# Kernel tuning notes

Hardware: AMD Instinct MI355X
Metric: run time of the kernel (lower is better)

## Reference

```python
import jax, jax.numpy as jnp
import numpy as np

LR, AT, DSBETA, EPS_DS = 0.3, 0.9, 1e-4, 0.01


def setup_inputs() -> dict:
    key = jax.random.key(0)
    k1, k2, k3, k4, k5 = jax.random.split(key, 5)
    B, K, D = 8192, 4096, 512
    # 0.25 scale -> squared distances small enough that act_max straddles the 0.9 threshold
    return {
        "input": jax.random.normal(k1, (B, D), jnp.float32) * 0.25,
        "weights": jax.random.normal(k2, (K, D), jnp.float32) * 0.25,
        "moving_avg": jax.random.uniform(k3, (K, D), jnp.float32),
        "relevance": jax.random.uniform(k4, (K, D), jnp.float32),
        "node_control": jax.random.randint(k5, (K,), 0, 2).astype(jnp.float32),
    }


def _forward(input, weights, moving_avg, relevance, node_control):
    B, D = input.shape
    K = weights.shape[0]
    # activation: relevance-weighted pairwise sq-distance
    rel_sum = relevance.sum(1)                                   # [K]
    d = ((input ** 2).sum(1)[:, None] + (weights ** 2).sum(1)[None, :]
         - 2.0 * input @ weights.T)                              # [B,K]
    dw = d * (rel_sum / D)[None, :]
    dw = jnp.where(jnp.isnan(dw), 0.0, dw)
    act = rel_sum[None, :] / (rel_sum[None, :] + dw + 1e-7)      # [B,K]
    act_max = act.max(1)
    idx = jnp.argmax(act, 1)                                     # BMU per sample
    high = act_max >= AT                                         # [B]

    # ---- high-activation branch: segment-mean EMA update of winning nodes ----
    hi = high.astype(input.dtype)
    cnt = jax.ops.segment_sum(hi, idx, num_segments=K)           # [K]
    sums = jax.ops.segment_sum(input * hi[:, None], idx, num_segments=K)
    upd = cnt > 0                                                # nodes that won >=1 high sample
    mean_k = sums / jnp.where(upd, cnt, 1.0)[:, None]            # per-node mean sample
    dist_abs = jnp.abs(mean_k - weights)
    a = LR * DSBETA
    ma1 = jnp.where(upd[:, None], a * dist_abs + (1.0 - a) * moving_avg, moving_avg)
    mx = ma1.max(1, keepdims=True)
    mn = ma1.min(1, keepdims=True)
    av = ma1.mean(1, keepdims=True)
    rel_new = 1.0 / (1.0 + jnp.exp((ma1 - av) / (EPS_DS * (mx - mn))))
    rel1 = jnp.where(upd[:, None], rel_new, relevance)
    delta = LR * (mean_k - weights)
    w1 = jnp.where(upd[:, None], weights + delta, weights)
    nc1 = jnp.where(upd, 1.0, node_control)
    loss = (delta * upd[:, None]).sum() / B

    # ---- low-activation branch: add_node -> copy segment means into free slots ----
    lo = (~high).astype(input.dtype)
    cnt_l = jax.ops.segment_sum(lo, idx, num_segments=K)
    sums_l = jax.ops.segment_sum(input * lo[:, None], idx, num_segments=K)
    low_valid = cnt_l > 0
    low_mean = sums_l / jnp.where(low_valid, cnt_l, 1.0)[:, None]
    avail = nc1 == 0
    n_new = low_valid.sum()
    n_avail = avail.sum()
    n_create = jnp.minimum(n_new, n_avail)
    # torch.unique returns sorted node ids; stable argsort puts valid ids first ascending
    low_order = jnp.argsort(jnp.where(low_valid, 0, 1))          # [K]
    avail_order = jnp.argsort(jnp.where(avail, 0, 1))            # [K]
    r = jnp.arange(K)
    # add_node takes the LAST n_create new samples, fills FIRST n_create free slots
    src = low_order[jnp.clip(n_new - n_create + r, 0, K - 1)]
    vals = low_mean[src]                                         # [K,D]
    wm = r < n_create                                            # write mask per rank
    slot = avail_order                                           # permutation of [K]
    w2 = w1.at[slot].set(jnp.where(wm[:, None], vals, w1[slot]))
    ma2 = ma1.at[slot].set(jnp.where(wm[:, None], 0.0, ma1[slot]))
    rel2 = rel1.at[slot].set(jnp.where(wm[:, None], 1.0, rel1[slot]))
    nc2 = nc1.at[slot].set(jnp.where(wm, 1.0, nc1[slot]))

    state = jnp.stack([w2, ma2, rel2], axis=0)                   # [3,K,D]
    return loss, state, nc2


def reference(input, weights, moving_avg, relevance, node_control):
    return _forward(input, weights, moving_avg, relevance, node_control)
```

## Files before the change

### kernel.cpp

```cpp
#include <hip/hip_runtime.h>

typedef unsigned short ushort_t;
typedef unsigned int uint_t;
typedef __bf16 bf16x8 __attribute__((ext_vector_type(8)));
typedef float f32x4 __attribute__((ext_vector_type(4)));

#define BM 128
#define BN 128

static constexpr float LRC  = 0.3f;
static constexpr float AC   = (float)(0.3 * 1e-4);
static constexpr float OMAC = (float)(1.0 - 0.3 * 1e-4);
static constexpr float EPSC = 0.01f;
static constexpr float ATC  = 0.9f;
static constexpr float DELTA = 5e-4f;

__device__ __forceinline__ void gll16(const void* g, void* l) {
    __builtin_amdgcn_global_load_lds((__attribute__((address_space(1))) void*)g,
                                     (__attribute__((address_space(3))) void*)l,
                                     16, 0, 0);
}

__device__ __forceinline__ ushort_t f2bf_rne(float f) {
    uint_t u = __float_as_uint(f);
    uint_t r = u + 0x7fffu + ((u >> 16) & 1u);
    return (ushort_t)(r >> 16);
}

__global__ __launch_bounds__(128) void k_prep(
    const float* __restrict__ X, const float* __restrict__ W,
    const float* __restrict__ REL,
    ushort_t* __restrict__ Xh, ushort_t* __restrict__ Wh,
    float* __restrict__ xsq, float* __restrict__ wsq, float* __restrict__ rel_sum,
    int B, int D)
{
    int blk = blockIdx.x, t = threadIdx.x;
    bool isX = blk < B;
    int row = isX ? blk : blk - B;
    const float4* src = (const float4*)((isX ? X : W) + (size_t)row * D);
    const float4* rr  = isX ? nullptr : (const float4*)(REL + (size_t)row * D);
    ushort_t* H = isX ? Xh : Wh;
    float q = 0.f, r = 0.f;
    for (int i = t; i < (D >> 2); i += 128) {
        float4 v = src[i];
        if (!isX) { float4 rv = rr[i]; r += rv.x + rv.y + rv.z + rv.w; }
        float x[4] = {v.x, v.y, v.z, v.w};
        ushort_t h[4];
#pragma unroll
        for (int j = 0; j < 4; j++) { q += x[j] * x[j]; h[j] = f2bf_rne(x[j]); }
        ((ushort4*)H)[(size_t)row * (D >> 2) + i] = make_ushort4(h[0], h[1], h[2], h[3]);
    }
    __shared__ float s1[128], s2[128];
    s1[t] = q; s2[t] = r; __syncthreads();
    for (int off = 64; off > 0; off >>= 1) {
        if (t < off) { s1[t] += s1[t + off]; s2[t] += s2[t + off]; }
        __syncthreads();
    }
    if (t == 0) {
        if (isX) xsq[row] = s1[0];
        else { wsq[row] = s1[0]; rel_sum[row] = s2[0]; }
    }
}

__global__ __launch_bounds__(256, 2) void k_gemm_act(
    const ushort_t* __restrict__ Xh, const ushort_t* __restrict__ Wh,
    const float* __restrict__ xsq, const float* __restrict__ wsq,
    const float* __restrict__ rs,
    float* __restrict__ tmaxA, int* __restrict__ cntA,
    float* __restrict__ actsA, int* __restrict__ idxsA,
    int K, int D)
{
    __shared__ char smem[26624];

    const int tid = threadIdx.x;
    const int wave = tid >> 6, lane = tid & 63;
    const int nk = K / BN;
    const int bx = blockIdx.x % nk, by = blockIdx.x / nk;
    const int b0 = by * BM, k0 = bx * BN;

    const int srow = wave * 32 + (lane >> 2);
    const int schunk = ((lane & 3) - (lane >> 3)) & 3;
    const int scol = schunk * 8;
    const size_t gx = (size_t)(b0 + srow) * D + scol;
    const size_t gw = (size_t)(k0 + srow) * D + scol;
    const size_t c1 = (size_t)16 * D;
    char* lb = smem + wave * 2048;

    const int wm = wave >> 1, wn = wave & 1;
    const int l15 = lane & 15, quad = lane >> 4;
    const int roff = (l15 * 4 + ((quad + (l15 >> 1)) & 3)) * 16;
    const int aoff = (wm * 4) * 1024 + roff;
    const int boff = (wn * 4) * 1024 + roff;

    f32x4 acc[4][4];
#pragma unroll
    for (int i = 0; i < 4; i++)
#pragma unroll
        for (int j = 0; j < 4; j++) acc[i][j] = (f32x4){0.f, 0.f, 0.f, 0.f};

    for (int kd = 0; kd < D; kd += 32) {
        gll16(Xh + gx + kd,      lb + 0);
        gll16(Xh + gx + c1 + kd, lb + 1024);
        gll16(Wh + gw + kd,      lb + 8192);
        gll16(Wh + gw + c1 + kd, lb + 8192 + 1024);
        __syncthreads();

        bf16x8 ah[4], bh[4];
#pragma unroll
        for (int t = 0; t < 4; t++) {
            ah[t] = *(const bf16x8*)(smem + 0    + aoff + t * 1024);
            bh[t] = *(const bf16x8*)(smem + 8192 + boff + t * 1024);
        }
#pragma unroll
        for (int j = 0; j < 4; j++)
#pragma unroll
            for (int i = 0; i < 4; i++)
                acc[i][j] = __builtin_amdgcn_mfma_f32_16x16x32_bf16(ah[i], bh[j], acc[i][j], 0, 0, 0);
        __syncthreads();
    }

    float rsv[4], wqv[4], epsors[4];
#pragma unroll
    for (int tn = 0; tn < 4; tn++) {
        int c = k0 + wn * 64 + tn * 16 + l15;
        float rv = rs[c];
        rsv[tn] = rv; wqv[tn] = wsq[c];
        epsors[tn] = 1e-7f / rv;
    }
    const float invD = 1.f / (float)D;
    float* redM    = (float*)smem;
    float* tmaxrow = (float*)(smem + 16896);
    float* thrqrow = (float*)(smem + 17408);
    int*   cntL    = (int*)(smem + 17920);
    float* lsActs  = (float*)(smem + 18432);
    int*   lsIdx   = (int*)(smem + 22528);

#pragma unroll
    for (int tm = 0; tm < 4; tm++) {
#pragma unroll
        for (int r = 0; r < 4; r++) {
            int rowl = wm * 64 + tm * 16 + quad * 4 + r;
            float xq = xsq[b0 + rowl];
            float qmin = 1e30f;
#pragma unroll
            for (int tn = 0; tn < 4; tn++) {
                float dd = (xq + wqv[tn]) - 2.f * acc[tm][tn][r];
                float q = dd * invD + epsors[tn];
                acc[tm][tn][r] = q;
                qmin = fminf(qmin, q);
            }
            redM[rowl * 33 + wn * 16 + l15] = qmin;
        }
    }
    __syncthreads();
    if (tid < BM) {
        float qm = 1e30f;
#pragma unroll
        for (int t2 = 0; t2 < 32; t2++) qm = fminf(qm, redM[tid * 33 + t2]);
        float tmax = 1.f / (1.f + qm);
        tmaxrow[tid] = tmax;
        thrqrow[tid] = 1.f / (tmax - DELTA) - 1.f;
        cntL[tid] = 0;
    }
    __syncthreads();
#pragma unroll
    for (int tm = 0; tm < 4; tm++) {
#pragma unroll
        for (int r = 0; r < 4; r++) {
            int rowl = wm * 64 + tm * 16 + quad * 4 + r;
            float tq = thrqrow[rowl];
#pragma unroll
            for (int tn = 0; tn < 4; tn++) {
                float q = acc[tm][tn][r];
                if (q <= tq) {
                    int pos = atomicAdd(&cntL[rowl], 1);
                    if (pos < 8) {
                        lsActs[rowl * 8 + pos] = 1.f / (1.f + q);
                        lsIdx[rowl * 8 + pos]  = k0 + wn * 64 + tn * 16 + l15;
                    }
                }
            }
        }
    }
    __syncthreads();
    if (tid < BM) {
        size_t base = (size_t)(b0 + tid) * nk + bx;
        tmaxA[base] = tmaxrow[tid];
        int c = cntL[tid];
        cntA[base] = c;
        int cc = c < 8 ? c : 8;
        for (int s = 0; s < cc; s++) {
            actsA[base * 8 + s] = lsActs[tid * 8 + s];
            idxsA[base * 8 + s] = lsIdx[tid * 8 + s];
        }
    }
}

__global__ __launch_bounds__(64) void k_refine(
    const float* __restrict__ X, const float* __restrict__ W,
    const float* __restrict__ xsq, const float* __restrict__ wsq,
    const float* __restrict__ rs,
    const float* __restrict__ tmaxA, const int* __restrict__ cntA,
    const float* __restrict__ actsA, const int* __restrict__ idxsA,
    int nk, int* __restrict__ cnt, int* __restrict__ cnt_l,
    int* __restrict__ idxb, int* __restrict__ rankb, int* __restrict__ highb,
    int K, int D)
{
    int b = blockIdx.x, ln = threadIdx.x;
    const float4* xp = (const float4*)(X + (size_t)b * D + ln * 8);
    float4 xa = xp[0], xb = xp[1];
    float xr[8] = {xa.x, xa.y, xa.z, xa.w, xb.x, xb.y, xb.z, xb.w};
    float xq = xsq[b];
    const float invD = 1.f / (float)D;

    float tmax = (ln < nk) ? tmaxA[(size_t)b * nk + ln] : -1e30f;
    int   tcnt = (ln < nk) ? cntA[(size_t)b * nk + ln] : 0;
    float M = tmax;
#pragma unroll
    for (int o = 32; o > 0; o >>= 1) M = fmaxf(M, __shfl_xor(M, o));
    float thr = M - DELTA;

    float best = -1e30f; int bidx = 0x7fffffff;

    auto exact_upd = [&](int idx) {
        const float* wr = W + (size_t)idx * D + ln * 8;
        float p = 0.f;
#pragma unroll
        for (int j = 0; j < 8; j++) p = fmaf(xr[j], wr[j], p);
#pragma unroll
        for (int o = 32; o > 0; o >>= 1) p += __shfl_xor(p, o);
        float rsv = rs[idx];
        float dd = (xq + wsq[idx]) - 2.f * p;
        float dw = dd * (rsv * invD);
        if (dw != dw) dw = 0.f;
        float act = rsv / ((rsv + dw) + 1e-7f);
        if (act > best || (act == best && idx < bidx)) { best = act; bidx = idx; }
    };

    for (int t = 0; t < nk; t++) {
        float tm = __shfl(tmax, t);
        int   tc = __shfl(tcnt, t);
        if (tm < thr) continue;
        if (tc <= 8) {
            size_t base = ((size_t)b * nk + t) * 8;
            for (int s = 0; s < tc; s++) {
                float aact = actsA[base + s];
                if (aact < thr) continue;
                exact_upd(idxsA[base + s]);
            }
        } else {
            for (int k2 = t * BN; k2 < t * BN + BN; k2++) exact_upd(k2);
        }
    }

    if (ln == 0) {
        int hi = (best >= ATC) ? 1 : 0;
        int rank = atomicAdd((hi ? cnt : cnt_l) + bidx, 1);
        idxb[b] = bidx; rankb[b] = rank; highb[b] = hi;
    }
}

__global__ __launch_bounds__(1024) void k_offsets(
    const int* __restrict__ cnt, const int* __restrict__ cnt_l,
    const float* __restrict__ NC,
    int* __restrict__ offs_h, int* __restrict__ offs_l,
    int* __restrict__ slot_src, int K)
{
    __shared__ int sA[1024], sB[1024];
    __shared__ int lowL[4096], availL[4096];
    int t = threadIdx.x;
    int per = (K + 1023) / 1024;
    int base = t * per;
    int ch[8], cl[8]; int sh = 0, sl = 0;
    for (int j = 0; j < per; j++) {
        int k = base + j;
        int a = (k < K) ? cnt[k] : 0;
        int b = (k < K) ? cnt_l[k] : 0;
        ch[j] = a; cl[j] = b; sh += a; sl += b;
    }
    sA[t] = sh; sB[t] = sl; __syncthreads();
    for (int off = 1; off < 1024; off <<= 1) {
        int vA = (t >= off) ? sA[t - off] : 0;
        int vB = (t >= off) ? sB[t - off] : 0;
        __syncthreads();
        sA[t] += vA; sB[t] += vB;
        __syncthreads();
    }
    int eh = sA[t] - sh, el = sB[t] - sl;
    for (int j = 0; j < per; j++) {
        int k = base + j;
        if (k < K) { offs_h[k] = eh; offs_l[k] = el; }
        eh += ch[j]; el += cl[j];
    }
    __syncthreads();
    int lv[8], av[8]; int cL = 0, cA = 0;
    for (int j = 0; j < per; j++) {
        int k = base + j;
        int l = 0, a = 0;
        if (k < K) {
            l = (cl[j] > 0) ? 1 : 0;
            float nc1 = (ch[j] > 0) ? 1.f : NC[k];
            a = (nc1 == 0.f) ? 1 : 0;
        }
        lv[j] = l; av[j] = a; cL += l; cA += a;
    }
    sA[t] = cL; sB[t] = cA; __syncthreads();
    for (int off = 1; off < 1024; off <<= 1) {
        int vA = (t >= off) ? sA[t - off] : 0;
        int vB = (t >= off) ? sB[t - off] : 0;
        __syncthreads();
        sA[t] += vA; sB[t] += vB;
        __syncthreads();
    }
    int totL = sA[1023], totA = sB[1023];
    int eL = sA[t] - cL, eA = sB[t] - cA;
    for (int j = 0; j < per; j++) {
        if (lv[j]) lowL[eL++] = base + j;
        if (av[j]) availL[eA++] = base + j;
    }
    for (int j = 0; j < per; j++) {
        int k = base + j;
        if (k < K) slot_src[k] = -1;
    }
    __syncthreads();
    int n_create = (totL < totA) ? totL : totA;
    for (int r = t; r < n_create; r += 1024)
        slot_src[availL[r]] = lowL[totL - n_create + r];
}

__global__ __launch_bounds__(256) void k_scatter(
    const int* __restrict__ idxb, const int* __restrict__ rankb,
    const int* __restrict__ highb,
    const int* __restrict__ offs_h, const int* __restrict__ offs_l,
    int* __restrict__ list_h, int* __restrict__ list_l, int B)
{
    int b = blockIdx.x * 256 + threadIdx.x;
    if (b >= B) return;
    int node = idxb[b];
    if (highb[b]) list_h[offs_h[node] + rankb[b]] = b;
    else          list_l[offs_l[node] + rankb[b]] = b;
}

__global__ __launch_bounds__(256) void k_final(
    const float* __restrict__ X,
    const float* __restrict__ W, const float* __restrict__ MA,
    const float* __restrict__ REL, const float* __restrict__ NC,
    const int* __restrict__ cnt, const int* __restrict__ offs_h,
    const int* __restrict__ list_h,
    const int* __restrict__ cnt_l, const int* __restrict__ offs_l,
    const int* __restrict__ list_l, const int* __restrict__ slot_src,
    float* __restrict__ outW, float* __restrict__ outMA,
    float* __restrict__ outREL, float* __restrict__ outNC,
    float* __restrict__ outLoss, int D, float invB)
{
    int k = blockIdx.x, t = threadIdx.x;
    size_t ro = (size_t)k * D;
    int t2 = t + 256;
    int src = slot_src[k];
    int n = cnt[k];
    __shared__ float rbuf[12];
    if (src >= 0) {
        int m = cnt_l[src];
        int base = offs_l[src];
        float s0 = 0.f, s1 = 0.f;
        for (int i = 0; i < m; i++) {
            int b = list_l[base + i];
            const float* xr = X + (size_t)b * D;
            s0 += xr[t]; s1 += xr[t2];
        }
        float fm = (float)m;
        outW[ro + t]  = s0 / fm; outW[ro + t2]  = s1 / fm;
        outMA[ro + t] = 0.f;     outMA[ro + t2] = 0.f;
        outREL[ro + t] = 1.f;    outREL[ro + t2] = 1.f;
        if (t == 0) outNC[k] = 1.f;
    } else if (n > 0) {
        float s0 = 0.f, s1 = 0.f;
        int base = offs_h[k];
        for (int i = 0; i < n; i++) {
            int b = list_h[base + i];
            const float* xr = X + (size_t)b * D;
            s0 += xr[t]; s1 += xr[t2];
        }
        float fn = (float)n;
        float mean0 = s0 / fn, mean1 = s1 / fn;
        float w0 = W[ro + t],  w1 = W[ro + t2];
        float a0 = MA[ro + t], a1 = MA[ro + t2];
        float m0 = AC * fabsf(mean0 - w0) + OMAC * a0;
        float m1 = AC * fabsf(mean1 - w1) + OMAC * a1;

        float vmax = fmaxf(m0, m1), vmin = fminf(m0, m1), vsum = m0 + m1;
#pragma unroll
        for (int o = 1; o < 64; o <<= 1) {
            vmax = fmaxf(vmax, __shfl_xor(vmax, o));
            vmin = fminf(vmin, __shfl_xor(vmin, o));
            vsum += __shfl_xor(vsum, o);
        }
        int wv = t >> 6, ln = t & 63;
        if (ln == 0) { rbuf[wv] = vmax; rbuf[4 + wv] = vmin; rbuf[8 + wv] = vsum; }
        __syncthreads();
        float mx = fmaxf(fmaxf(rbuf[0], rbuf[1]), fmaxf(rbuf[2], rbuf[3]));
        float mn = fminf(fminf(rbuf[4], rbuf[5]), fminf(rbuf[6], rbuf[7]));
        float av = (rbuf[8] + rbuf[9] + rbuf[10] + rbuf[11]) / (float)D;

        float scale = EPSC * (mx - mn);
        float r0 = 1.f / (1.f + expf((m0 - av) / scale));
        float r1 = 1.f / (1.f + expf((m1 - av) / scale));
        float d0 = LRC * (mean0 - w0), d1 = LRC * (mean1 - w1);

        outW[ro + t]  = w0 + d0;  outW[ro + t2]  = w1 + d1;
        outMA[ro + t] = m0;       outMA[ro + t2] = m1;
        outREL[ro + t] = r0;      outREL[ro + t2] = r1;

        float ls = d0 + d1;
#pragma unroll
        for (int o = 1; o < 64; o <<= 1) ls += __shfl_xor(ls, o);
        __syncthreads();
        if (ln == 0) rbuf[wv] = ls;
        __syncthreads();
        if (t == 0) {
            atomicAdd(outLoss, (rbuf[0] + rbuf[1] + rbuf[2] + rbuf[3]) * invB);
            outNC[k] = 1.f;
        }
    } else {
        outW[ro + t]  = W[ro + t];   outW[ro + t2]  = W[ro + t2];
        outMA[ro + t] = MA[ro + t];  outMA[ro + t2] = MA[ro + t2];
        outREL[ro + t] = REL[ro + t]; outREL[ro + t2] = REL[ro + t2];
        if (t == 0) outNC[k] = NC[k];
    }
}

extern "C" void kernel_launch(void* const* d_in, const int* in_sizes, int n_in,
                              void* d_out, int out_size, void* d_ws, size_t ws_size,
                              hipStream_t stream) {
    const float* X   = (const float*)d_in[0];
    const float* W   = (const float*)d_in[1];
    const float* MA  = (const float*)d_in[2];
    const float* REL = (const float*)d_in[3];
    const float* NC  = (const float*)d_in[4];

    const int K = in_sizes[4];
    const int D = in_sizes[1] / K;
    const int B = in_sizes[0] / D;
    const int NKT = K / BN;
    const size_t KD = (size_t)K * D;
    const size_t BD = (size_t)B * D;

    float* out = (float*)d_out;
    float* outLoss = out;
    float* outW   = out + 1;
    float* outMA  = out + 1 + KD;
    float* outREL = out + 1 + 2 * KD;
    float* outNC  = out + 1 + 3 * KD;

    float* wsf = (float*)d_ws;
    size_t off = 0;
    ushort_t* Xh = (ushort_t*)(wsf + off); off += BD / 2;
    ushort_t* Wh = (ushort_t*)(wsf + off); off += KD / 2;
    float* rel_sum = wsf + off; off += K;
    float* wsq     = wsf + off; off += K;
    float* xsq     = wsf + off; off += B;
    float* tmaxA   = wsf + off; off += (size_t)B * NKT;
    int*   cntA    = (int*)(wsf + off); off += (size_t)B * NKT;
    float* actsA   = wsf + off; off += (size_t)B * NKT * 8;
    int*   idxsA   = (int*)(wsf + off); off += (size_t)B * NKT * 8;
    int*   idxb    = (int*)(wsf + off); off += B;
    int*   rankb   = (int*)(wsf + off); off += B;
    int*   highb   = (int*)(wsf + off); off += B;
    int*   list_h  = (int*)(wsf + off); off += B;
    int*   list_l  = (int*)(wsf + off); off += B;
    int*   offs_h  = (int*)(wsf + off); off += K;
    int*   offs_l  = (int*)(wsf + off); off += K;
    int*   slot_src = (int*)(wsf + off); off += K;
    int*   cnt     = (int*)(wsf + off); off += K;
    int*   cnt_l   = (int*)(wsf + off); off += K;

    hipMemsetAsync(cnt, 0, 2 * (size_t)K * sizeof(int), stream);
    hipMemsetAsync(outLoss, 0, sizeof(float), stream);

    k_prep<<<B + K, 128, 0, stream>>>(X, W, REL, Xh, Wh, xsq, wsq, rel_sum, B, D);
    k_gemm_act<<<(B / BM) * (K / BN), 256, 0, stream>>>(Xh, Wh, xsq, wsq, rel_sum,
                                                        tmaxA, cntA, actsA, idxsA,
                                                        K, D);
    k_refine<<<B, 64, 0, stream>>>(X, W, xsq, wsq, rel_sum,
                                   tmaxA, cntA, actsA, idxsA, NKT,
                                   cnt, cnt_l, idxb, rankb, highb, K, D);
    k_offsets<<<1, 1024, 0, stream>>>(cnt, cnt_l, NC, offs_h, offs_l,
                                      slot_src, K);
    k_scatter<<<(B + 255) / 256, 256, 0, stream>>>(idxb, rankb, highb,
                                                   offs_h, offs_l,
                                                   list_h, list_l, B);
    k_final<<<K, 256, 0, stream>>>(X, W, MA, REL, NC, cnt, offs_h, list_h,
                                   cnt_l, offs_l, list_l, slot_src,
                                   outW, outMA, outREL, outNC, outLoss,
                                   D, 1.f / (float)B);
}
```

Baseline: 251.6 us.

## Fold memsets into prep kernel, wave-level scans, one wave per node in final

Drops the two hipMemsetAsync calls by zeroing the counters and loss inside k_prep. Replaces the block-wide shared-memory Hillis-Steele scans in k_offsets with wave shuffle scans plus a small per-wave sum table. Restructures k_final so each 64-lane wave handles one node with 8 floats per lane (vectorised loads and stores), which removes block barriers and the shared reduction buffer. The aim is fewer launches and less synchronisation overhead. Because k_final now hardcodes 8 floats per lane, it assumes D equals 512.

```diff
diff --git a/kernel.cpp b/kernel.cpp
--- a/kernel.cpp
+++ b/kernel.cpp
@@ -32,11 +32,14 @@
     const float* __restrict__ REL,
     ushort_t* __restrict__ Xh, ushort_t* __restrict__ Wh,
     float* __restrict__ xsq, float* __restrict__ wsq, float* __restrict__ rel_sum,
+    int* __restrict__ cnt, int* __restrict__ cnt_l, float* __restrict__ outLoss,
     int B, int D)
 {
     int blk = blockIdx.x, t = threadIdx.x;
     bool isX = blk < B;
     int row = isX ? blk : blk - B;
+    if (blk == 0 && t == 0) *outLoss = 0.f;
+    if (!isX && t == 0) { cnt[row] = 0; cnt_l[row] = 0; }
     const float4* src = (const float4*)((isX ? X : W) + (size_t)row * D);
     const float4* rr  = isX ? nullptr : (const float4*)(REL + (size_t)row * D);
     ushort_t* H = isX ? Xh : Wh;
@@ -266,11 +269,12 @@
     int* __restrict__ offs_h, int* __restrict__ offs_l,
     int* __restrict__ slot_src, int K)
 {
-    __shared__ int sA[1024], sB[1024];
+    __shared__ int wsumA[16], wsumB[16];
     __shared__ int lowL[4096], availL[4096];
-    int t = threadIdx.x;
+    int t = threadIdx.x, ln = t & 63, wv = t >> 6;
     int per = (K + 1023) / 1024;
     int base = t * per;
+
     int ch[8], cl[8]; int sh = 0, sl = 0;
     for (int j = 0; j < per; j++) {
         int k = base + j;
@@ -278,21 +282,24 @@
         int b = (k < K) ? cnt_l[k] : 0;
         ch[j] = a; cl[j] = b; sh += a; sl += b;
     }
-    sA[t] = sh; sB[t] = sl; __syncthreads();
-    for (int off = 1; off < 1024; off <<= 1) {
-        int vA = (t >= off) ? sA[t - off] : 0;
-        int vB = (t >= off) ? sB[t - off] : 0;
-        __syncthreads();
-        sA[t] += vA; sB[t] += vB;
-        __syncthreads();
-    }
-    int eh = sA[t] - sh, el = sB[t] - sl;
+    int ia = sh, ib = sl;
+#pragma unroll
+    for (int o = 1; o < 64; o <<= 1) {
+        int ua = __shfl_up(ia, o), ub = __shfl_up(ib, o);
+        if (ln >= o) { ia += ua; ib += ub; }
+    }
+    if (ln == 63) { wsumA[wv] = ia; wsumB[wv] = ib; }
+    __syncthreads();
+    int woA = 0, woB = 0;
+    for (int i = 0; i < wv; i++) { woA += wsumA[i]; woB += wsumB[i]; }
+    int eh = woA + ia - sh, el = woB + ib - sl;
     for (int j = 0; j < per; j++) {
         int k = base + j;
         if (k < K) { offs_h[k] = eh; offs_l[k] = el; }
         eh += ch[j]; el += cl[j];
     }
     __syncthreads();
+
     int lv[8], av[8]; int cL = 0, cA = 0;
     for (int j = 0; j < per; j++) {
         int k = base + j;
@@ -304,16 +311,21 @@
         }
         lv[j] = l; av[j] = a; cL += l; cA += a;
     }
-    sA[t] = cL; sB[t] = cA; __syncthreads();
-    for (int off = 1; off < 1024; off <<= 1) {
-        int vA = (t >= off) ? sA[t - off] : 0;
-        int vB = (t >= off) ? sB[t - off] : 0;
-        __syncthreads();
-        sA[t] += vA; sB[t] += vB;
-        __syncthreads();
-    }
-    int totL = sA[1023], totA = sB[1023];
-    int eL = sA[t] - cL, eA = sB[t] - cA;
+    ia = cL; ib = cA;
+#pragma unroll
+    for (int o = 1; o < 64; o <<= 1) {
+        int ua = __shfl_up(ia, o), ub = __shfl_up(ib, o);
+        if (ln >= o) { ia += ua; ib += ub; }
+    }
+    if (ln == 63) { wsumA[wv] = ia; wsumB[wv] = ib; }
+    __syncthreads();
+    woA = 0; woB = 0;
+    int totL = 0, totA = 0;
+    for (int i = 0; i < 16; i++) {
+        if (i < wv) { woA += wsumA[i]; woB += wsumB[i]; }
+        totL += wsumA[i]; totA += wsumB[i];
+    }
+    int eL = woA + ia - cL, eA = woB + ib - cA;
     for (int j = 0; j < per; j++) {
         if (lv[j]) lowL[eL++] = base + j;
         if (av[j]) availL[eA++] = base + j;
@@ -351,81 +363,92 @@
     const int* __restrict__ list_l, const int* __restrict__ slot_src,
     float* __restrict__ outW, float* __restrict__ outMA,
     float* __restrict__ outREL, float* __restrict__ outNC,
-    float* __restrict__ outLoss, int D, float invB)
+    float* __restrict__ outLoss, int K, int D, float invB)
 {
-    int k = blockIdx.x, t = threadIdx.x;
-    size_t ro = (size_t)k * D;
-    int t2 = t + 256;
+    int k = (blockIdx.x * 256 + threadIdx.x) >> 6;
+    int ln = threadIdx.x & 63;
+    if (k >= K) return;
+    size_t ro = (size_t)k * D + ln * 8;
     int src = slot_src[k];
     int n = cnt[k];
-    __shared__ float rbuf[12];
+
     if (src >= 0) {
         int m = cnt_l[src];
         int base = offs_l[src];
-        float s0 = 0.f, s1 = 0.f;
+        f32x4 s0 = {0.f,0.f,0.f,0.f}, s1 = {0.f,0.f,0.f,0.f};
         for (int i = 0; i < m; i++) {
             int b = list_l[base + i];
-            const float* xr = X + (size_t)b * D;
-            s0 += xr[t]; s1 += xr[t2];
+            const f32x4* xr = (const f32x4*)(X + (size_t)b * D + ln * 8);
+            s0 += xr[0]; s1 += xr[1];
         }
         float fm = (float)m;
-        outW[ro + t]  = s0 / fm; outW[ro + t2]  = s1 / fm;
-        outMA[ro + t] = 0.f;     outMA[ro + t2] = 0.f;
-        outREL[ro + t] = 1.f;    outREL[ro + t2] = 1.f;
-        if (t == 0) outNC[k] = 1.f;
+        f32x4 one = {1.f,1.f,1.f,1.f}, zero = {0.f,0.f,0.f,0.f};
+#pragma unroll
+        for (int j = 0; j < 4; j++) { s0[j] /= fm; s1[j] /= fm; }
+        ((f32x4*)(outW + ro))[0] = s0;  ((f32x4*)(outW + ro))[1] = s1;
+        ((f32x4*)(outMA + ro))[0] = zero; ((f32x4*)(outMA + ro))[1] = zero;
+        ((f32x4*)(outREL + ro))[0] = one; ((f32x4*)(outREL + ro))[1] = one;
+        if (ln == 0) outNC[k] = 1.f;
     } else if (n > 0) {
-        float s0 = 0.f, s1 = 0.f;
         int base = offs_h[k];
+        f32x4 s0 = {0.f,0.f,0.f,0.f}, s1 = {0.f,0.f,0.f,0.f};
         for (int i = 0; i < n; i++) {
             int b = list_h[base + i];
-            const float* xr = X + (size_t)b * D;
-            s0 += xr[t]; s1 += xr[t2];
+            const f32x4* xr = (const f32x4*)(X + (size_t)b * D + ln * 8);
+            s0 += xr[0]; s1 += xr[1];
         }
         float fn = (float)n;
-        float mean0 = s0 / fn, mean1 = s1 / fn;
-        float w0 = W[ro + t],  w1 = W[ro + t2];
-        float a0 = MA[ro + t], a1 = MA[ro + t2];
-        float m0 = AC * fabsf(mean0 - w0) + OMAC * a0;
-        float m1 = AC * fabsf(mean1 - w1) + OMAC * a1;
-
-        float vmax = fmaxf(m0, m1), vmin = fminf(m0, m1), vsum = m0 + m1;
+        f32x4 wv0 = ((const f32x4*)(W + ro))[0],  wv1 = ((const f32x4*)(W + ro))[1];
+        f32x4 av0 = ((const f32x4*)(MA + ro))[0], av1 = ((const f32x4*)(MA + ro))[1];
+        float mean[8], w[8], m[8], d[8];
+#pragma unroll
+        for (int j = 0; j < 4; j++) {
+            mean[j]     = s0[j] / fn;  mean[j + 4] = s1[j] / fn;
+            w[j] = wv0[j]; w[j + 4] = wv1[j];
+            m[j]     = AC * fabsf(mean[j] - w[j]) + OMAC * av0[j];
+            m[j + 4] = AC * fabsf(mean[j + 4] - w[j + 4]) + OMAC * av1[j];
+        }
+        float vmax = m[0], vmin = m[0], vsum = 0.f;
+#pragma unroll
+        for (int j = 0; j < 8; j++) {
+            vmax = fmaxf(vmax, m[j]); vmin = fminf(vmin, m[j]); vsum += m[j];
+        }
 #pragma unroll
         for (int o = 1; o < 64; o <<= 1) {
             vmax = fmaxf(vmax, __shfl_xor(vmax, o));
             vmin = fminf(vmin, __shfl_xor(vmin, o));
             vsum += __shfl_xor(vsum, o);
         }
-        int wv = t >> 6, ln = t & 63;
-        if (ln == 0) { rbuf[wv] = vmax; rbuf[4 + wv] = vmin; rbuf[8 + wv] = vsum; }
-        __syncthreads();
-        float mx = fmaxf(fmaxf(rbuf[0], rbuf[1]), fmaxf(rbuf[2], rbuf[3]));
-        float mn = fminf(fminf(rbuf[4], rbuf[5]), fminf(rbuf[6], rbuf[7]));
-        float av = (rbuf[8] + rbuf[9] + rbuf[10] + rbuf[11]) / (float)D;
-
-        float scale = EPSC * (mx - mn);
-        float r0 = 1.f / (1.f + expf((m0 - av) / scale));
-        float r1 = 1.f / (1.f + expf((m1 - av) / scale));
-        float d0 = LRC * (mean0 - w0), d1 = LRC * (mean1 - w1);
-
-        outW[ro + t]  = w0 + d0;  outW[ro + t2]  = w1 + d1;
-        outMA[ro + t] = m0;       outMA[ro + t2] = m1;
-        outREL[ro + t] = r0;      outREL[ro + t2] = r1;
-
-        float ls = d0 + d1;
+        float av = vsum / (float)D;
+        float iscale = 1.f / (EPSC * (vmax - vmin));
+        f32x4 mo0, mo1, ro0, ro1, wo0, wo1;
+        float ls = 0.f;
+#pragma unroll
+        for (int j = 0; j < 8; j++) {
+            float r = 1.f / (1.f + expf((m[j] - av) * iscale));
+            d[j] = LRC * (mean[j] - w[j]);
+            ls += d[j];
+            float wn = w[j] + d[j];
+            if (j < 4) { mo0[j] = m[j]; ro0[j] = r; wo0[j] = wn; }
+            else       { mo1[j-4] = m[j]; ro1[j-4] = r; wo1[j-4] = wn; }
+        }
+        ((f32x4*)(outW + ro))[0] = wo0;  ((f32x4*)(outW + ro))[1] = wo1;
+        ((f32x4*)(outMA + ro))[0] = mo0; ((f32x4*)(outMA + ro))[1] = mo1;
+        ((f32x4*)(outREL + ro))[0] = ro0; ((f32x4*)(outREL + ro))[1] = ro1;
 #pragma unroll
         for (int o = 1; o < 64; o <<= 1) ls += __shfl_xor(ls, o);
-        __syncthreads();
-        if (ln == 0) rbuf[wv] = ls;
-        __syncthreads();
-        if (t == 0) {
-            atomicAdd(outLoss, (rbuf[0] + rbuf[1] + rbuf[2] + rbuf[3]) * invB);
+        if (ln == 0) {
+            atomicAdd(outLoss, ls * invB);
             outNC[k] = 1.f;
         }
     } else {
-        outW[ro + t]  = W[ro + t];   outW[ro + t2]  = W[ro + t2];
-        outMA[ro + t] = MA[ro + t];  outMA[ro + t2] = MA[ro + t2];
-        outREL[ro + t] = REL[ro + t]; outREL[ro + t2] = REL[ro + t2];
-        if (t == 0) outNC[k] = NC[k];
+        f32x4 a0 = ((const f32x4*)(W + ro))[0],  a1 = ((const f32x4*)(W + ro))[1];
+        f32x4 b0 = ((const f32x4*)(MA + ro))[0], b1 = ((const f32x4*)(MA + ro))[1];
+        f32x4 c0 = ((const f32x4*)(REL + ro))[0], c1 = ((const f32x4*)(REL + ro))[1];
+        ((f32x4*)(outW + ro))[0] = a0;  ((f32x4*)(outW + ro))[1] = a1;
+        ((f32x4*)(outMA + ro))[0] = b0; ((f32x4*)(outMA + ro))[1] = b1;
+        ((f32x4*)(outREL + ro))[0] = c0; ((f32x4*)(outREL + ro))[1] = c1;
+        if (ln == 0) outNC[k] = NC[k];
     }
 }
 
@@ -474,10 +497,8 @@
     int*   cnt     = (int*)(wsf + off); off += K;
     int*   cnt_l   = (int*)(wsf + off); off += K;
 
-    hipMemsetAsync(cnt, 0, 2 * (size_t)K * sizeof(int), stream);
-    hipMemsetAsync(outLoss, 0, sizeof(float), stream);
-
-    k_prep<<<B + K, 128, 0, stream>>>(X, W, REL, Xh, Wh, xsq, wsq, rel_sum, B, D);
+    k_prep<<<B + K, 128, 0, stream>>>(X, W, REL, Xh, Wh, xsq, wsq, rel_sum,
+                                      cnt, cnt_l, outLoss, B, D);
     k_gemm_act<<<(B / BM) * (K / BN), 256, 0, stream>>>(Xh, Wh, xsq, wsq, rel_sum,
                                                         tmaxA, cntA, actsA, idxsA,
                                                         K, D);
@@ -489,8 +510,8 @@
     k_scatter<<<(B + 255) / 256, 256, 0, stream>>>(idxb, rankb, highb,
                                                    offs_h, offs_l,
                                                    list_h, list_l, B);
-    k_final<<<K, 256, 0, stream>>>(X, W, MA, REL, NC, cnt, offs_h, list_h,
-                                   cnt_l, offs_l, list_l, slot_src,
-                                   outW, outMA, outREL, outNC, outLoss,
-                                   D, 1.f / (float)B);
-}
+    k_final<<<K / 4, 256, 0, stream>>>(X, W, MA, REL, NC, cnt, offs_h, list_h,
+                                       cnt_l, offs_l, list_l, slot_src,
+                                       outW, outMA, outREL, outNC, outLoss,
+                                       K, D, 1.f / (float)B);
+}
```

Result: no change. 253.8 us (+0.9%).
